# Kernel tuning notes

Measured on AMD Instinct MI355X. Metric: run time of the kernel, lower is better.

Reference implementation:

```python
import jax, jax.numpy as jnp
import numpy as np

TEMP = 1.0  # composition softmax temperature

def _bank_topk(x, U, V, logits, top_k):
    # softmax over primitive logits, select top-k, renormalize, fused low-rank projection
    w = jax.nn.softmax(logits / TEMP)                     # [P]
    tw, ti = jax.lax.top_k(w, top_k)                      # [k], [k]
    tw = tw / tw.sum()
    Us = U[ti]                                            # [k, d_in, r]
    Vs = V[ti]                                            # [k, r, d_out]
    h = jnp.einsum('bsd,kdr->bksr', x, Us)                # low-rank bottleneck
    return jnp.einsum('bksr,kro,k->bso', h, Vs, tw)       # weighted fuse

def reference(x, q_U, q_V, k_U, k_V, v_U, v_V, q_logits, k_logits, v_logits, out_w, top_k):
    B, S, _ = x.shape
    H, D = 16, 64
    q = _bank_topk(x, q_U, q_V, q_logits, top_k)
    k = _bank_topk(x, k_U, k_V, k_logits, top_k)
    v = _bank_topk(x, v_U, v_V, v_logits, top_k)
    q = q.reshape(B, S, H, D).transpose(0, 2, 1, 3)       # [B,H,S,D]
    k = k.reshape(B, S, H, D).transpose(0, 2, 1, 3)
    v = v.reshape(B, S, H, D).transpose(0, 2, 1, 3)
    scale = 1.0 / jnp.sqrt(jnp.asarray(D, dtype=x.dtype))
    scores = jnp.einsum('bhqd,bhkd->bhqk', q, k) * scale  # [B,H,S,S]
    causal = jnp.triu(jnp.ones((S, S), dtype=bool), 1)
    scores = jnp.where(causal[None, None], jnp.finfo(x.dtype).min, scores)
    probs = jax.nn.softmax(scores, axis=-1)
    out = jnp.einsum('bhqk,bhkd->bhqd', probs, v)
    out = out.transpose(0, 2, 1, 3).reshape(B, S, H * D)
    return out @ out_w.T                                   # nn.Linear(H*D, d_model, bias=False)

def setup_inputs() -> dict:
    key = jax.random.key(0)
    ks = jax.random.split(key, 11)
    P, d, r = 16, 1024, 64
    B, S = 4, 1024
    f = jnp.float32
    inp = {
        'x': jax.random.normal(ks[0], (B, S, d), f),
        'q_U': jax.random.normal(ks[1], (P, d, r), f) * (1.0 / np.sqrt(d)),
        'q_V': jax.random.normal(ks[2], (P, r, d), f) * (1.0 / np.sqrt(r)),
        'k_U': jax.random.normal(ks[3], (P, d, r), f) * (1.0 / np.sqrt(d)),
        'k_V': jax.random.normal(ks[4], (P, r, d), f) * (1.0 / np.sqrt(r)),
        'v_U': jax.random.normal(ks[5], (P, d, r), f) * (1.0 / np.sqrt(d)),
        'v_V': jax.random.normal(ks[6], (P, r, d), f) * (1.0 / np.sqrt(r)),
        'q_logits': jax.random.normal(ks[7], (P,), f) * 0.01,
        'k_logits': jax.random.normal(ks[8], (P,), f) * 0.01,
        'v_logits': jax.random.normal(ks[9], (P,), f) * 0.01,
        'out_w': jax.random.normal(ks[10], (d, d), f) * (1.0 / np.sqrt(d)),
        'top_k': 4,
    }
    return inp
```

## Files before the change

kernel.cpp:

```cpp
#include <hip/hip_runtime.h>
#include <math.h>

#define D_MODEL 1024
#define RANK    64
#define PMAX    16
#define S_LEN   1024
#define HD      64
#define MROWS   4096
#define NHEAD   16
#define BATCH   4
#define KCMAX   (PMAX * RANK)

typedef short short8v __attribute__((ext_vector_type(8)));
typedef short short4v __attribute__((ext_vector_type(4)));
typedef float floatx4 __attribute__((ext_vector_type(4)));

typedef __attribute__((address_space(1))) const unsigned int* gptr_t;
typedef __attribute__((address_space(3))) unsigned int* lptr_t;
typedef __attribute__((address_space(3))) short* lds3s;

static __device__ __forceinline__ void async16(const void* g, void* l) {
    __builtin_amdgcn_global_load_lds((gptr_t)g, (lptr_t)l, 16, 0, 0);
}

static __device__ __forceinline__ short f2bf(float f) {
    unsigned int u = __float_as_uint(f);
    u = (u + 0x7fffu + ((u >> 16) & 1u)) >> 16;
    return (short)u;
}

__global__ __launch_bounds__(256) void convert_bf16_kernel(
    const float* __restrict__ x, short* __restrict__ xb,
    const float* __restrict__ w, short* __restrict__ wb) {
    int i = blockIdx.x * 256 + threadIdx.x;
    const int NX = MROWS * D_MODEL / 4;
    const int NW = D_MODEL * D_MODEL / 4;
    const float* src;
    short* dst;
    if (i < NX) {
        src = x; dst = xb;
    } else {
        i -= NX;
        if (i >= NW) return;
        src = w; dst = wb;
    }
    float4 f = ((const float4*)src)[i];
    short4 o;
    o.x = f2bf(f.x); o.y = f2bf(f.y); o.z = f2bf(f.z); o.w = f2bf(f.w);
    ((short4*)dst)[i] = o;
}

__global__ __launch_bounds__(256) void prep_uv_kernel(
    const float* __restrict__ qU, const float* __restrict__ kU,
    const float* __restrict__ vU,
    const float* __restrict__ qV, const float* __restrict__ kV,
    const float* __restrict__ vV,
    const float* __restrict__ ql, const float* __restrict__ kl,
    const float* __restrict__ vl,
    const int* __restrict__ topk,
    short* __restrict__ Uc, short* __restrict__ Vt) {
    int z    = blockIdx.z;
    int j    = blockIdx.y;
    int tile = blockIdx.x;
    int t    = threadIdx.x;
    int K = *topk; if (K < 1) K = 1; if (K > PMAX) K = PMAX;
    if (j >= K) return;
    __shared__ float T[64][65];
    int bank = (z < 3) ? z : z - 3;

    const float* lg = (bank == 0) ? ql : (bank == 1) ? kl : vl;
    float l[PMAX];
    bool used[PMAX];
    for (int i = 0; i < PMAX; ++i) { l[i] = lg[i]; used[i] = false; }
    int   si[PMAX];
    float sl[PMAX];
    for (int jj = 0; jj < K; ++jj) {
        int best = -1; float bv = -INFINITY;
        for (int i = 0; i < PMAX; ++i)
            if (!used[i] && l[i] > bv) { bv = l[i]; best = i; }
        used[best] = true; si[jj] = best; sl[jj] = bv;
    }
    float mx = sl[0], sum = 0.f, ej = 0.f;
    for (int jj = 0; jj < K; ++jj) {
        float e = __expf(sl[jj] - mx);
        sum += e;
        if (jj == j) ej = e;
    }
    int   p  = si[j];
    float wj = ej / sum;

    if (z < 3) {
        const float* U = (bank == 0) ? qU : (bank == 1) ? kU : vU;
        const float* src = U + (size_t)p * D_MODEL * RANK;
        short* dst = Uc + (size_t)bank * D_MODEL * KCMAX;
        int r4 = (t & 15) * 4;
        int dl = t >> 4;
#pragma unroll
        for (int i = 0; i < 4; ++i) {
            int d = tile * 64 + i * 16 + dl;
            float4 f = *(const float4*)&src[(size_t)d * RANK + r4];
            short4 o;
            o.x = f2bf(f.x); o.y = f2bf(f.y); o.z = f2bf(f.z); o.w = f2bf(f.w);
            *(short4*)&dst[(size_t)d * KCMAX + j * 64 + r4] = o;
        }
    } else {
        const float* V = (bank == 0) ? qV : (bank == 1) ? kV : vV;
        const float* src = V + (size_t)p * RANK * D_MODEL;
        int n0 = tile * 64;
        int nl = t & 63, rq = t >> 6;
#pragma unroll
        for (int i = 0; i < 16; ++i) {
            int rl = i * 4 + rq;
            T[nl][rl] = src[(size_t)rl * D_MODEL + n0 + nl] * wj;
        }
        __syncthreads();
        short* dst = Vt + (size_t)bank * D_MODEL * KCMAX;
        int rr = t >> 2;
#pragma unroll
        for (int i = 0; i < 4; ++i) {
            int c = (t & 3) * 16 + i * 4;
            short4 o;
            o.x = f2bf(T[rr][c + 0]); o.y = f2bf(T[rr][c + 1]);
            o.z = f2bf(T[rr][c + 2]); o.w = f2bf(T[rr][c + 3]);
            *(short4*)&dst[(size_t)(n0 + rr) * KCMAX + j * 64 + c] = o;
        }
    }
}

static __device__ __forceinline__ void mfma_gemm_tile(
    const short* __restrict__ A, const short* __restrict__ B, int kl,
    int lda, int ldb, int m0, int n0, short* As, short* Bs, floatx4 acc[4][4]) {
    const int t    = threadIdx.x;
    const int w    = t >> 6;
    const int lane = t & 63;
    const int wm   = w & 1, wn = w >> 1;
    const int colL = lane & 15, quad = lane >> 4;
    const int srow  = lane >> 2;
    const int skoff = (lane & 3) * 8;

#pragma unroll
    for (int i = 0; i < 4; ++i)
#pragma unroll
        for (int j = 0; j < 4; ++j) acc[i][j] = (floatx4){0.f, 0.f, 0.f, 0.f};

    for (int k0 = 0; k0 < kl; k0 += 32) {
        async16(A + (size_t)(m0 + w * 16 + srow) * lda + k0 + skoff,
                As + (w * 16 + srow) * 32 + skoff);
        async16(A + (size_t)(m0 + 64 + w * 16 + srow) * lda + k0 + skoff,
                As + (64 + w * 16 + srow) * 32 + skoff);
        async16(B + (size_t)(n0 + w * 16 + srow) * ldb + k0 + skoff,
                Bs + (w * 16 + srow) * 32 + skoff);
        async16(B + (size_t)(n0 + 64 + w * 16 + srow) * ldb + k0 + skoff,
                Bs + (64 + w * 16 + srow) * 32 + skoff);
        __syncthreads();
        short8v af[4], bf[4];
#pragma unroll
        for (int i = 0; i < 4; ++i)
            af[i] = *(const short8v*)&As[(wm * 64 + i * 16 + colL) * 32 + quad * 8];
#pragma unroll
        for (int j = 0; j < 4; ++j)
            bf[j] = *(const short8v*)&Bs[(wn * 64 + j * 16 + colL) * 32 + quad * 8];
#pragma unroll
        for (int i = 0; i < 4; ++i)
#pragma unroll
            for (int j = 0; j < 4; ++j)
                acc[i][j] = __builtin_amdgcn_mfma_f32_16x16x32_bf16(af[i], bf[j], acc[i][j], 0, 0, 0);
        __syncthreads();
    }
}

__global__ __launch_bounds__(256) void gemm_weff_kernel(
    const short* __restrict__ Vt, const short* __restrict__ Uc,
    const int* __restrict__ topk, short* __restrict__ Wt) {
    int K = *topk; if (K < 1) K = 1; if (K > PMAX) K = PMAX;
    int id = blockIdx.x + 8 * (blockIdx.y + 8 * blockIdx.z);
    int sw = (id & 7) * 24 + (id >> 3);
    int m0 = (sw & 7) * 128; int rest = sw >> 3;
    int n0 = (rest & 7) * 128; int bank = rest >> 3;
    __shared__ short As[128 * 32];
    __shared__ short Bs[128 * 32];
    floatx4 acc[4][4];
    mfma_gemm_tile(Vt + (size_t)bank * D_MODEL * KCMAX,
                   Uc + (size_t)bank * D_MODEL * KCMAX,
                   K * 64, KCMAX, KCMAX, m0, n0, As, Bs, acc);

    const int t = threadIdx.x, w = t >> 6, lane = t & 63;
    const int wm = w & 1, wn = w >> 1, colL = lane & 15, quad = lane >> 4;
    short* Wb = Wt + (size_t)bank * D_MODEL * D_MODEL;
#pragma unroll
    for (int i = 0; i < 4; ++i)
#pragma unroll
        for (int j = 0; j < 4; ++j)
#pragma unroll
            for (int r = 0; r < 4; ++r)
                Wb[(size_t)(m0 + wm * 64 + i * 16 + quad * 4 + r) * D_MODEL +
                   (n0 + wn * 64 + j * 16 + colL)] = f2bf(acc[i][j][r]);
}

__global__ __launch_bounds__(256) void gemm_qkv_kernel(
    const short* __restrict__ xb, const short* __restrict__ Wt,
    short* __restrict__ qkv) {
    int id = blockIdx.x + 32 * (blockIdx.y + 8 * blockIdx.z);
    int sw = (id & 7) * 96 + (id >> 3);
    int m0 = (sw & 31) * 128; int rest = sw >> 5;
    int n0 = (rest & 7) * 128; int bank = rest >> 3;
    __shared__ short As[128 * 32];
    __shared__ short Bs[128 * 32];
    floatx4 acc[4][4];
    mfma_gemm_tile(xb, Wt + (size_t)bank * D_MODEL * D_MODEL,
                   D_MODEL, D_MODEL, D_MODEL, m0, n0, As, Bs, acc);

    const int t = threadIdx.x, w = t >> 6, lane = t & 63;
    const int wm = w & 1, wn = w >> 1, colL = lane & 15, quad = lane >> 4;
    short* outp = qkv + (size_t)bank * MROWS * D_MODEL;
#pragma unroll
    for (int i = 0; i < 4; ++i)
#pragma unroll
        for (int j = 0; j < 4; ++j)
#pragma unroll
            for (int r = 0; r < 4; ++r) {
                int m = m0 + wm * 64 + i * 16 + quad * 4 + r;
                int n = n0 + wn * 64 + j * 16 + colL;
                int b = m >> 10, s = m & 1023;
                int head = n >> 6, d = n & 63;
                outp[(((size_t)(b * NHEAD + head) << 10) + s) * HD + d] = f2bf(acc[i][j][r]);
            }
}

__global__ __launch_bounds__(256) void gemm_proj_kernel(
    const short* __restrict__ attnb, const short* __restrict__ wb,
    float* __restrict__ outp) {
    int id = blockIdx.x + 32 * blockIdx.y;
    int sw = (id & 7) * 32 + (id >> 3);
    int m0 = (sw & 31) * 128;
    int n0 = (sw >> 5) * 128;
    __shared__ short As[128 * 32];
    __shared__ short Bs[128 * 32];
    floatx4 acc[4][4];
    mfma_gemm_tile(attnb, wb, D_MODEL, D_MODEL, D_MODEL, m0, n0, As, Bs, acc);

    const int t = threadIdx.x, w = t >> 6, lane = t & 63;
    const int wm = w & 1, wn = w >> 1, colL = lane & 15, quad = lane >> 4;
#pragma unroll
    for (int i = 0; i < 4; ++i)
#pragma unroll
        for (int j = 0; j < 4; ++j)
#pragma unroll
            for (int r = 0; r < 4; ++r)
                outp[(size_t)(m0 + wm * 64 + i * 16 + quad * 4 + r) * D_MODEL +
                     (n0 + wn * 64 + j * 16 + colL)] = acc[i][j][r];
}

__global__ __launch_bounds__(256) void attn_mfma_kernel(
    const short* __restrict__ qkv,
    short* __restrict__ attn_out) {
    const int t    = threadIdx.x;
    const int w    = t >> 6;
    const int lane = t & 63;
    const int col  = lane & 15;
    const int quad = lane >> 4;
    int id = blockIdx.x + 8 * blockIdx.y;
    int swz = (id & 7) * 64 + (id >> 3);
    const int pr = swz & 7;
    const int bh = swz >> 3;
    const size_t HS   = (size_t)S_LEN * HD;
    const size_t BSTR = (size_t)MROWS * D_MODEL;
    const short* Qg = qkv + (size_t)bh * HS;
    const short* Kg = qkv + BSTR + (size_t)bh * HS;
    const short* Vg = qkv + 2 * BSTR + (size_t)bh * HS;

    __shared__ short Ks[2][128 * 64];
    __shared__ short Vs[2][128 * 64];

    const float SC = 0.125f * 1.44269504f;

    int krow[4], kslot[4], vkey[4], voff[4];
#pragma unroll
    for (int it = 0; it < 4; ++it) {
        int c = t + it * 256;
        krow[it]  = c >> 3;
        kslot[it] = (c & 7) ^ ((c >> 3) & 7);
        int h = c & 1, kr = (c >> 1) & 3, k4 = (c >> 3) & 31, d16 = c >> 8;
        vkey[it] = k4 * 4 + kr;
        voff[it] = d16 * 16 + h * 8;
    }
    const int sw0 = (quad ^ (col & 7)) * 16;
    const int sw1 = ((4 + quad) ^ (col & 7)) * 16;
    lds3s vb = (lds3s)&Vs[0][quad * 64 + col * 4];

    auto STAGE = [&](int buf, int jt) {
#pragma unroll
        for (int it = 0; it < 4; ++it) {
            async16(Kg + (size_t)(jt * 128 + krow[it]) * HD + kslot[it] * 8,
                    &Ks[buf][(t + it * 256) * 8]);
            async16(Vg + (size_t)(jt * 128 + vkey[it]) * HD + voff[it],
                    &Vs[buf][(t + it * 256) * 8]);
        }
    };

    for (int ph = 0; ph < 2; ++ph) {
        const int qt = ph ? (15 - pr) : pr;
        const int qb = qt * 4 + w;
        const int qrow = qt * 64 + w * 16 + col;
        short8v aq0 = *(const short8v*)(Qg + (size_t)qrow * HD + quad * 8);
        short8v aq1 = *(const short8v*)(Qg + (size_t)qrow * HD + 32 + quad * 8);
        asm volatile("s_waitcnt vmcnt(0)" : "+v"(aq0), "+v"(aq1) :: "memory");
        floatx4 O0 = {0.f, 0.f, 0.f, 0.f}, O1 = O0, O2 = O0, O3 = O0;
        float mrow = -INFINITY, lrow = 0.f;
        const int nkv = (qt + 2) >> 1;

        STAGE(0, 0);
        int cur = 0;
        for (int jt = 0; jt < nkv; ++jt) {
            __builtin_amdgcn_sched_barrier(0);
            if (jt + 1 < nkv) {
                STAGE(cur ^ 1, jt + 1);
                asm volatile("s_waitcnt vmcnt(8)" ::: "memory");
            } else {
                asm volatile("s_waitcnt vmcnt(0)" ::: "memory");
            }
            __builtin_amdgcn_s_barrier();
            __builtin_amdgcn_sched_barrier(0);

            const short* Kb = &Ks[cur][0];
            lds3s vbc = vb + cur * (128 * 64);

            const int base = jt * 8;
            float s[8][4];
#pragma unroll
            for (int mb = 0; mb < 8; ++mb) {
                int rel = qb - (base + mb);
                if (rel >= 0) {
                    floatx4 c4 = {0.f, 0.f, 0.f, 0.f};
                    const char* kp = (const char*)Kb + mb * 2048 + col * 128;
                    short8v a0 = *(const short8v*)(kp + sw0);
                    short8v a1 = *(const short8v*)(kp + sw1);
                    c4 = __builtin_amdgcn_mfma_f32_16x16x32_bf16(a0, aq0, c4, 0, 0, 0);
                    c4 = __builtin_amdgcn_mfma_f32_16x16x32_bf16(a1, aq1, c4, 0, 0, 0);
#pragma unroll
                    for (int r = 0; r < 4; ++r) {
                        float v = c4[r] * SC;
                        if (rel == 0 && quad * 4 + r > col) v = -INFINITY;
                        s[mb][r] = v;
                    }
                } else {
#pragma unroll
                    for (int r = 0; r < 4; ++r) s[mb][r] = -INFINITY;
                }
            }
            float tm = -INFINITY;
#pragma unroll
            for (int mb = 0; mb < 8; ++mb)
#pragma unroll
                for (int r = 0; r < 4; ++r) tm = fmaxf(tm, s[mb][r]);
            tm = fmaxf(tm, __shfl_xor(tm, 16));
            tm = fmaxf(tm, __shfl_xor(tm, 32));
            if (__any(tm > mrow + 8.0f)) {
                float mnew  = fmaxf(mrow, tm);
                float alpha = exp2f(mrow - mnew);
                lrow *= alpha;
                mrow = mnew;
#pragma unroll
                for (int r = 0; r < 4; ++r) {
                    float ar = __shfl(alpha, quad * 4 + r);
                    O0[r] *= ar; O1[r] *= ar; O2[r] *= ar; O3[r] *= ar;
                }
            }
            float p[8][4];
            float ps = 0.f;
#pragma unroll
            for (int mb = 0; mb < 8; ++mb)
#pragma unroll
                for (int r = 0; r < 4; ++r) {
                    float e = exp2f(s[mb][r] - mrow);
                    p[mb][r] = e; ps += e;
                }
            ps += __shfl_xor(ps, 16);
            ps += __shfl_xor(ps, 32);
            lrow += ps;

            int lim = qb * 16 + 15 - (jt << 7);
            int ksm = lim >> 5; if (ksm > 3) ksm = 3;
#pragma unroll
            for (int ks = 0; ks < 4; ++ks) {
                if (ks <= ksm) {
                    lds3s vc = vbc + ks * 512;
                    short4v t00, t01, t10, t11, t20, t21, t30, t31;
                    asm volatile("ds_read_b64_tr_b16 %0, %1" : "=v"(t00) : "v"(vc));
                    asm volatile("ds_read_b64_tr_b16 %0, %1" : "=v"(t01) : "v"(vc + 256));
                    asm volatile("ds_read_b64_tr_b16 %0, %1" : "=v"(t10) : "v"(vc + 2048));
                    asm volatile("ds_read_b64_tr_b16 %0, %1" : "=v"(t11) : "v"(vc + 2304));
                    asm volatile("ds_read_b64_tr_b16 %0, %1" : "=v"(t20) : "v"(vc + 4096));
                    asm volatile("ds_read_b64_tr_b16 %0, %1" : "=v"(t21) : "v"(vc + 4352));
                    asm volatile("ds_read_b64_tr_b16 %0, %1" : "=v"(t30) : "v"(vc + 6144));
                    asm volatile("ds_read_b64_tr_b16 %0, %1" : "=v"(t31) : "v"(vc + 6400));
                    short8v ap;
                    ap[0] = f2bf(p[2 * ks][0]);     ap[1] = f2bf(p[2 * ks][1]);
                    ap[2] = f2bf(p[2 * ks][2]);     ap[3] = f2bf(p[2 * ks][3]);
                    ap[4] = f2bf(p[2 * ks + 1][0]); ap[5] = f2bf(p[2 * ks + 1][1]);
                    ap[6] = f2bf(p[2 * ks + 1][2]); ap[7] = f2bf(p[2 * ks + 1][3]);
                    asm volatile("s_waitcnt lgkmcnt(0)" ::: "memory");
                    __builtin_amdgcn_sched_barrier(0);
                    short8v bv0 = __builtin_shufflevector(t00, t01, 0, 1, 2, 3, 4, 5, 6, 7);
                    short8v bv1 = __builtin_shufflevector(t10, t11, 0, 1, 2, 3, 4, 5, 6, 7);
                    short8v bv2 = __builtin_shufflevector(t20, t21, 0, 1, 2, 3, 4, 5, 6, 7);
                    short8v bv3 = __builtin_shufflevector(t30, t31, 0, 1, 2, 3, 4, 5, 6, 7);
                    O0 = __builtin_amdgcn_mfma_f32_16x16x32_bf16(ap, bv0, O0, 0, 0, 0);
                    O1 = __builtin_amdgcn_mfma_f32_16x16x32_bf16(ap, bv1, O1, 0, 0, 0);
                    O2 = __builtin_amdgcn_mfma_f32_16x16x32_bf16(ap, bv2, O2, 0, 0, 0);
                    O3 = __builtin_amdgcn_mfma_f32_16x16x32_bf16(ap, bv3, O3, 0, 0, 0);
                }
            }
            __builtin_amdgcn_sched_barrier(0);
            __builtin_amdgcn_s_barrier();
            cur ^= 1;
        }
        const int b  = bh >> 4;
        const int hh = bh & 15;
        short* orow = attn_out +
            ((size_t)(b * S_LEN) + qt * 64 + w * 16) * D_MODEL + hh * 64;
        float linv = 1.f / lrow;
#pragma unroll
        for (int r = 0; r < 4; ++r) {
            float inv = __shfl(linv, quad * 4 + r);
            short* prw = orow + (size_t)(quad * 4 + r) * D_MODEL;
            prw[0  + col] = f2bf(O0[r] * inv);
            prw[16 + col] = f2bf(O1[r] * inv);
            prw[32 + col] = f2bf(O2[r] * inv);
            prw[48 + col] = f2bf(O3[r] * inv);
        }
    }
}

extern "C" void kernel_launch(void* const* d_in, const int* in_sizes, int n_in,
                              void* d_out, int out_size, void* d_ws, size_t ws_size,
                              hipStream_t stream) {
    const float* x    = (const float*)d_in[0];
    const float* qU   = (const float*)d_in[1];
    const float* qV   = (const float*)d_in[2];
    const float* kU   = (const float*)d_in[3];
    const float* kV   = (const float*)d_in[4];
    const float* vU   = (const float*)d_in[5];
    const float* vV   = (const float*)d_in[6];
    const float* qlg  = (const float*)d_in[7];
    const float* klg  = (const float*)d_in[8];
    const float* vlg  = (const float*)d_in[9];
    const float* outw = (const float*)d_in[10];
    const int*   topk = (const int*)d_in[11];
    float* outp = (float*)d_out;

    char* ws = (char*)d_ws;
    short* xb   = (short*)(ws + 512);
    short* Uc   = xb + (size_t)MROWS * D_MODEL;
    short* Vt   = Uc + (size_t)3 * D_MODEL * KCMAX;
    short* wb   = Vt + (size_t)3 * D_MODEL * KCMAX;
    short* Wt   = wb + (size_t)D_MODEL * D_MODEL;
    short* qkvb = Wt + (size_t)3 * D_MODEL * D_MODEL;
    short* attnb = qkvb + (size_t)3 * MROWS * D_MODEL;

    const int NCV = (MROWS * D_MODEL + D_MODEL * D_MODEL) / 4 / 256;
    convert_bf16_kernel<<<NCV, 256, 0, stream>>>(x, xb, outw, wb);
    prep_uv_kernel<<<dim3(16, 16, 6), 256, 0, stream>>>(
        qU, kU, vU, qV, kV, vV, qlg, klg, vlg, topk, Uc, Vt);
    gemm_weff_kernel<<<dim3(8, 8, 3), 256, 0, stream>>>(Vt, Uc, topk, Wt);
    gemm_qkv_kernel<<<dim3(32, 8, 3), 256, 0, stream>>>(xb, Wt, qkvb);
    attn_mfma_kernel<<<dim3(8, 64), 256, 0, stream>>>(qkvb, attnb);
    gemm_proj_kernel<<<dim3(32, 8), 256, 0, stream>>>(attnb, wb, outp);
}
```

Before: 227.8 us.

## Merge conversion and prep kernels; single-buffer attention K/V staging

Merges the bf16 conversion kernel and the U/V prep kernel into one front kernel launch, which saves one kernel launch. The attention kernel drops its double-buffered K/V LDS staging in favour of a single buffer loaded synchronously between two __syncthreads each tile. This halves LDS use, which could raise occupancy, but it gives up the overlap of loads with compute and adds a barrier per tile.

After: 219.8 us. 3.5% less time.

```diff
diff --git a/kernel.cpp b/kernel.cpp
--- a/kernel.cpp
+++ b/kernel.cpp
@@ -10,6 +10,7 @@
 #define NHEAD   16
 #define BATCH   4
 #define KCMAX   (PMAX * RANK)
+#define NCVBLK  5120
 
 typedef short short8v __attribute__((ext_vector_type(8)));
 typedef short short4v __attribute__((ext_vector_type(4)));
@@ -29,28 +30,9 @@
     return (short)u;
 }
 
-__global__ __launch_bounds__(256) void convert_bf16_kernel(
-    const float* __restrict__ x, short* __restrict__ xb,
-    const float* __restrict__ w, short* __restrict__ wb) {
-    int i = blockIdx.x * 256 + threadIdx.x;
-    const int NX = MROWS * D_MODEL / 4;
-    const int NW = D_MODEL * D_MODEL / 4;
-    const float* src;
-    short* dst;
-    if (i < NX) {
-        src = x; dst = xb;
-    } else {
-        i -= NX;
-        if (i >= NW) return;
-        src = w; dst = wb;
-    }
-    float4 f = ((const float4*)src)[i];
-    short4 o;
-    o.x = f2bf(f.x); o.y = f2bf(f.y); o.z = f2bf(f.z); o.w = f2bf(f.w);
-    ((short4*)dst)[i] = o;
-}
-
-__global__ __launch_bounds__(256) void prep_uv_kernel(
+__global__ __launch_bounds__(256) void front_kernel(
+    const float* __restrict__ x,  short* __restrict__ xb,
+    const float* __restrict__ ow, short* __restrict__ wb,
     const float* __restrict__ qU, const float* __restrict__ kU,
     const float* __restrict__ vU,
     const float* __restrict__ qV, const float* __restrict__ kV,
@@ -59,14 +41,31 @@
     const float* __restrict__ vl,
     const int* __restrict__ topk,
     short* __restrict__ Uc, short* __restrict__ Vt) {
-    int z    = blockIdx.z;
-    int j    = blockIdx.y;
-    int tile = blockIdx.x;
-    int t    = threadIdx.x;
+    const int bid = blockIdx.x;
+    const int t   = threadIdx.x;
+    __shared__ float T[64][65];
+
+    if (bid < NCVBLK) {
+        int i = bid * 256 + t;
+        const int NX = MROWS * D_MODEL / 4;
+        const float* src;
+        short* dst;
+        if (i < NX) { src = x; dst = xb; }
+        else        { i -= NX; src = ow; dst = wb; }
+        float4 f = ((const float4*)src)[i];
+        short4 o;
+        o.x = f2bf(f.x); o.y = f2bf(f.y); o.z = f2bf(f.z); o.w = f2bf(f.w);
+        ((short4*)dst)[i] = o;
+        return;
+    }
+
+    const int id2  = bid - NCVBLK;
+    const int tile = id2 & 15;
+    const int j    = (id2 >> 4) & 15;
+    const int z    = id2 >> 8;
     int K = *topk; if (K < 1) K = 1; if (K > PMAX) K = PMAX;
     if (j >= K) return;
-    __shared__ float T[64][65];
-    int bank = (z < 3) ? z : z - 3;
+    const int bank = (z < 3) ? z : z - 3;
 
     const float* lg = (bank == 0) ? ql : (bank == 1) ? kl : vl;
     float l[PMAX];
@@ -86,8 +85,8 @@
         sum += e;
         if (jj == j) ej = e;
     }
-    int   p  = si[j];
-    float wj = ej / sum;
+    const int   p  = si[j];
+    const float wj = ej / sum;
 
     if (z < 3) {
         const float* U = (bank == 0) ? qU : (bank == 1) ? kU : vU;
@@ -269,8 +268,8 @@
     const short* Kg = qkv + BSTR + (size_t)bh * HS;
     const short* Vg = qkv + 2 * BSTR + (size_t)bh * HS;
 
-    __shared__ short Ks[2][128 * 64];
-    __shared__ short Vs[2][128 * 64];
+    __shared__ short Ks[128 * 64];
+    __shared__ short Vs[128 * 64];
 
     const float SC = 0.125f * 1.44269504f;
 
@@ -286,17 +285,7 @@
     }
     const int sw0 = (quad ^ (col & 7)) * 16;
     const int sw1 = ((4 + quad) ^ (col & 7)) * 16;
-    lds3s vb = (lds3s)&Vs[0][quad * 64 + col * 4];
-
-    auto STAGE = [&](int buf, int jt) {
-#pragma unroll
-        for (int it = 0; it < 4; ++it) {
-            async16(Kg + (size_t)(jt * 128 + krow[it]) * HD + kslot[it] * 8,
-                    &Ks[buf][(t + it * 256) * 8]);
-            async16(Vg + (size_t)(jt * 128 + vkey[it]) * HD + voff[it],
-                    &Vs[buf][(t + it * 256) * 8]);
-        }
-    };
+    lds3s vb = (lds3s)&Vs[quad * 64 + col * 4];
 
     for (int ph = 0; ph < 2; ++ph) {
         const int qt = ph ? (15 - pr) : pr;
@@ -304,26 +293,20 @@
         const int qrow = qt * 64 + w * 16 + col;
         short8v aq0 = *(const short8v*)(Qg + (size_t)qrow * HD + quad * 8);
         short8v aq1 = *(const short8v*)(Qg + (size_t)qrow * HD + 32 + quad * 8);
-        asm volatile("s_waitcnt vmcnt(0)" : "+v"(aq0), "+v"(aq1) :: "memory");
         floatx4 O0 = {0.f, 0.f, 0.f, 0.f}, O1 = O0, O2 = O0, O3 = O0;
         float mrow = -INFINITY, lrow = 0.f;
         const int nkv = (qt + 2) >> 1;
 
-        STAGE(0, 0);
-        int cur = 0;
         for (int jt = 0; jt < nkv; ++jt) {
-            __builtin_amdgcn_sched_barrier(0);
-            if (jt + 1 < nkv) {
-                STAGE(cur ^ 1, jt + 1);
-                asm volatile("s_waitcnt vmcnt(8)" ::: "memory");
-            } else {
-                asm volatile("s_waitcnt vmcnt(0)" ::: "memory");
+            __syncthreads();
+#pragma unroll
+            for (int it = 0; it < 4; ++it) {
+                async16(Kg + (size_t)(jt * 128 + krow[it]) * HD + kslot[it] * 8,
+                        Ks + (t + it * 256) * 8);
+                async16(Vg + (size_t)(jt * 128 + vkey[it]) * HD + voff[it],
+                        Vs + (t + it * 256) * 8);
             }
-            __builtin_amdgcn_s_barrier();
-            __builtin_amdgcn_sched_barrier(0);
-
-            const short* Kb = &Ks[cur][0];
-            lds3s vbc = vb + cur * (128 * 64);
+            __syncthreads();
 
             const int base = jt * 8;
             float s[8][4];
@@ -332,7 +315,7 @@
                 int rel = qb - (base + mb);
                 if (rel >= 0) {
                     floatx4 c4 = {0.f, 0.f, 0.f, 0.f};
-                    const char* kp = (const char*)Kb + mb * 2048 + col * 128;
+                    const char* kp = (const char*)Ks + mb * 2048 + col * 128;
                     short8v a0 = *(const short8v*)(kp + sw0);
                     short8v a1 = *(const short8v*)(kp + sw1);
                     c4 = __builtin_amdgcn_mfma_f32_16x16x32_bf16(a0, aq0, c4, 0, 0, 0);
@@ -384,7 +367,7 @@
 #pragma unroll
             for (int ks = 0; ks < 4; ++ks) {
                 if (ks <= ksm) {
-                    lds3s vc = vbc + ks * 512;
+                    lds3s vc = vb + ks * 512;
                     short4v t00, t01, t10, t11, t20, t21, t30, t31;
                     asm volatile("ds_read_b64_tr_b16 %0, %1" : "=v"(t00) : "v"(vc));
                     asm volatile("ds_read_b64_tr_b16 %0, %1" : "=v"(t01) : "v"(vc + 256));
@@ -411,9 +394,6 @@
                     O3 = __builtin_amdgcn_mfma_f32_16x16x32_bf16(ap, bv3, O3, 0, 0, 0);
                 }
             }
-            __builtin_amdgcn_sched_barrier(0);
-            __builtin_amdgcn_s_barrier();
-            cur ^= 1;
         }
         const int b  = bh >> 4;
         const int hh = bh & 15;
@@ -458,10 +438,8 @@
     short* qkvb = Wt + (size_t)3 * D_MODEL * D_MODEL;
     short* attnb = qkvb + (size_t)3 * MROWS * D_MODEL;
 
-    const int NCV = (MROWS * D_MODEL + D_MODEL * D_MODEL) / 4 / 256;
-    convert_bf16_kernel<<<NCV, 256, 0, stream>>>(x, xb, outw, wb);
-    prep_uv_kernel<<<dim3(16, 16, 6), 256, 0, stream>>>(
-        qU, kU, vU, qV, kV, vV, qlg, klg, vlg, topk, Uc, Vt);
+    front_kernel<<<NCVBLK + 16 * 16 * 6, 256, 0, stream>>>(
+        x, xb, outw, wb, qU, kU, vU, qV, kV, vV, qlg, klg, vlg, topk, Uc, Vt);
     gemm_weff_kernel<<<dim3(8, 8, 3), 256, 0, stream>>>(Vt, Uc, topk, Wt);
     gemm_qkv_kernel<<<dim3(32, 8, 3), 256, 0, stream>>>(xb, Wt, qkvb);
     attn_mfma_kernel<<<dim3(8, 64), 256, 0, stream>>>(qkvb, attnb);
```
